# Optimization experiments

Measured on AMD Instinct MI355X. Metric: run time of the kernel, lower is better.

The kernel has to match this reference:

```python
import jax, jax.numpy as jnp
import numpy as np

B = 524288
D_IN = 128
H = 16          # hard-coded by amax slicing in MLSTMCell
D_OUT = 4


def _quant(x, amax):
    # torch quant_tensor: clamp(round(x * 127/amax), -127, 127) -> int8 (kept as
    # integer-valued float32 here; exact since |v| <= 127)
    if amax.ndim > 1:
        amax = jnp.squeeze(amax, 1)
    return jnp.clip(jnp.round(x * (127.0 / amax)), -127.0, 127.0)


def _dequant(x, amax, double=False):
    max_range = 127.0 ** 2 if double else 127.0
    scale = max_range / amax
    if scale.ndim > 1:
        scale = jnp.squeeze(scale, 1)
    return x / scale


def setup_inputs() -> dict:
    key = jax.random.key(0)
    ks = jax.random.split(key, 13)
    # weights are stored pre-quantized int8 (integer-valued); torch casts them
    # to int32 before matmul, so integer-valued float32 is bit-exact in fp32
    intw = lambda k, shp: jax.random.randint(k, shp, -127, 128).astype(jnp.float32)
    x = jax.random.normal(ks[0], (B, D_IN), dtype=jnp.float32)
    h = jax.random.normal(ks[1], (B, H), dtype=jnp.float32) * 0.1
    c = jax.random.normal(ks[2], (B, H), dtype=jnp.float32) * 0.1
    w1 = intw(ks[3], (H, D_IN))          # net.0.weight
    w_ih = intw(ks[4], (4 * H, H))       # lstm.weight_ih
    w_hh = intw(ks[5], (4 * H, H))       # lstm.weight_hh
    w_out = intw(ks[6], (D_OUT, H))      # output_layer.weight
    u = lambda k, shp, lo, hi: jax.random.uniform(k, shp, minval=lo, maxval=hi, dtype=jnp.float32)
    amax_in0 = u(ks[7], (), 1.0, 4.0)            # net.0._input_quantizer._amax (per-tensor)
    amax_w0 = u(ks[8], (H, 1), 32.0, 127.0)      # net.0._weight_quantizer._amax (per-channel)
    amax_lstm_in = u(ks[9], (), 1.0, 4.0)        # lstm._input_quantizer._amax
    amax_w_lstm = u(ks[10], (4 * H, 1), 32.0, 127.0)  # lstm._weight_quantizer._amax
    amax_out_in = u(ks[11], (), 1.0, 4.0)        # output_layer._input_quantizer._amax
    amax_w_out = u(ks[12], (D_OUT, 1), 32.0, 127.0)   # output_layer._weight_quantizer._amax
    return dict(x=x, h=h, c=c, w1=w1, w_ih=w_ih, w_hh=w_hh, w_out=w_out,
                amax_in0=amax_in0, amax_w0=amax_w0, amax_lstm_in=amax_lstm_in,
                amax_w_lstm=amax_w_lstm, amax_out_in=amax_out_in, amax_w_out=amax_w_out)


def reference(x, h, c, w1, w_ih, w_hh, w_out, amax_in0, amax_w0,
              amax_lstm_in, amax_w_lstm, amax_out_in, amax_w_out):
    # --- fc_1: quantize input, int matmul, relu, requantize for lstm ---
    xq = _quant(x, amax_in0)                     # [B, D_IN] int8-valued
    a = xq @ w1.T                                # [B, H] int32-valued (exact in fp32)
    a = jnp.maximum(a, 0.0)                      # relu
    a = _quant(_dequant(a, amax_in0 * amax_w0, double=True), amax_lstm_in)  # [B, H]
    # --- quantize hidden state (hc arrives as float) ---
    hq = _quant(h, amax_lstm_in)
    cq = _quant(c, amax_lstm_in)
    # --- MLSTMCell ---
    amax = amax_lstm_in * amax_w_lstm            # [4H, 1]
    gates = a @ w_ih.T + hq @ w_hh.T             # [B, 4H] int32-valued
    gates = _dequant(gates, amax, double=True)
    i, f, g, o = jnp.split(gates, 4, axis=1)
    gates = jnp.concatenate([jax.nn.sigmoid(i), jax.nn.sigmoid(f),
                             jnp.tanh(g), jax.nn.sigmoid(o)], axis=1)
    gq = _quant(gates, amax)                     # [B, 4H] int8-valued
    i, f, g, o = jnp.split(gq, 4, axis=1)
    cy = (_dequant(f * cq, amax[16:32] * 3.4764, double=True)
          + _dequant(i * g, amax[:16] * amax[32:48], double=True))
    od = _dequant(o, amax[48:], double=False)
    hy = od * jnp.tanh(cy)
    # --- output layer ---
    xo = _quant(hy, amax_out_in) @ w_out.T       # [B, D_OUT]
    xo = _dequant(xo, amax_out_in * amax_w_out, double=True)
    return xo, hy, cy
```

## Files before the change

### kernel.cpp

```cpp
#include <hip/hip_runtime.h>
#include <math.h>
#include <limits.h>


#define OFF_QS    0
#define OFF_SFC1  4
#define OFF_SG    20
#define OFF_QG    84
#define OFF_SCF   148
#define OFF_SCIG  164
#define OFF_SOD   180
#define OFF_SXO   196
#define OFF_VBG   200
#define OFF_TI    216
#define OFF_TF    280
#define OFF_TO    344
#define OFF_TG    408
#define OFF_IGT   536
#define OFF_ODT   1064
#define OFF_W1P   1192
#define OFF_WIHP  1704
#define OFF_WHHP  1960
#define OFF_WOUTP 2216

__device__ __forceinline__ float qclip(float v) {
    return fminf(fmaxf(v, -127.0f), 127.0f);
}

__device__ __forceinline__ int sdot4(int a, int b, int c) {
#if __has_builtin(__builtin_amdgcn_sdot4)
    return __builtin_amdgcn_sdot4(a, b, c, false);
#else
    c += ((a << 24) >> 24) * ((b << 24) >> 24);
    c += ((a << 16) >> 24) * ((b << 16) >> 24);
    c += ((a << 8)  >> 24) * ((b << 8)  >> 24);
    c += (a >> 24) * (b >> 24);
    return c;
#endif
}

__device__ __forceinline__ int pack4i(int a, int b, int c, int d) {
    return (a & 255) | ((b & 255) << 8) | ((c & 255) << 16) | (d << 24);
}

__device__ __forceinline__ int pack4f(const float* p) {
    return pack4i((int)p[0], (int)p[1], (int)p[2], (int)p[3]);
}

typedef __attribute__((address_space(1))) const void g_void;
typedef __attribute__((address_space(3))) void l_void;

__device__ __forceinline__ void stage16(const float* g, float* l) {
    __builtin_amdgcn_global_load_lds((g_void*)g, (l_void*)l, 16, 0, 0);
}

#define WAIT_VM0()   { asm volatile("s_waitcnt vmcnt(0)" ::: "memory"); __builtin_amdgcn_sched_barrier(0); }
#define WAIT_VM4()   { asm volatile("s_waitcnt vmcnt(4)" ::: "memory"); __builtin_amdgcn_sched_barrier(0); }
#define WAIT_LGKM0() { asm volatile("s_waitcnt lgkmcnt(0)" ::: "memory"); __builtin_amdgcn_sched_barrier(0); }

__device__ __forceinline__ int qeval_sig(int gi, float s, float q) {
    float v = (float)gi / s;
    float a = 1.0f / (1.0f + expf(-v));
    return (int)qclip(rintf(a * q));
}
__device__ __forceinline__ int qeval_tanh(int gi, float s, float q) {
    float v = (float)gi / s;
    float a = tanhf(v);
    return (int)qclip(rintf(a * q));
}

#define GLIM 1048576

__device__ int search_thr_sig(float s, float q, int target) {
    if (qeval_sig(GLIM, s, q) < target) return INT_MAX;
    int lo = -GLIM, hi = GLIM;
    while (hi - lo > 1) {
        int mid = lo + ((hi - lo) >> 1);
        if (qeval_sig(mid, s, q) >= target) hi = mid; else lo = mid;
    }
    return hi;
}
__device__ int search_thr_tanh(float s, float q, int target) {
    if (qeval_tanh(GLIM, s, q) < target) return INT_MAX;
    int lo = -GLIM, hi = GLIM;
    while (hi - lo > 1) {
        int mid = lo + ((hi - lo) >> 1);
        if (qeval_tanh(mid, s, q) >= target) hi = mid; else lo = mid;
    }
    return hi;
}

__global__ void __launch_bounds__(1024) setup_all(
    const float* __restrict__ w1, const float* __restrict__ w_ih,
    const float* __restrict__ w_hh, const float* __restrict__ w_out,
    const float* __restrict__ a_in0, const float* __restrict__ a_w0,
    const float* __restrict__ a_lstm, const float* __restrict__ a_wl,
    const float* __restrict__ a_out, const float* __restrict__ a_wo,
    float* __restrict__ wsf)
{
    const int t = threadIdx.x;
    int* wsi = (int*)wsf;
    const float amax_in0 = a_in0[0], amax_lstm = a_lstm[0], amax_out = a_out[0];

    if (t == 0) {
        wsf[OFF_QS + 0] = 127.0f / amax_in0;
        wsf[OFF_QS + 1] = 127.0f / amax_lstm;
        wsf[OFF_QS + 2] = 127.0f / amax_out;
    }
    if (t < 16) wsf[OFF_SFC1 + t] = 16129.0f / (amax_in0 * a_w0[t]);
    if (t < 64) {
        float am = amax_lstm * a_wl[t];
        wsf[OFF_SG + t] = 16129.0f / am;
        wsf[OFF_QG + t] = 127.0f / am;
    }
    if (t < 16) {
        float amf = amax_lstm * a_wl[16 + t];
        wsf[OFF_SCF + t] = 16129.0f / (amf * 3.4764f);
        float amo = amax_lstm * a_wl[48 + t];
        wsf[OFF_SOD + t] = 127.0f / amo;
        float ami = amax_lstm * a_wl[t];
        float amg = amax_lstm * a_wl[32 + t];
        wsf[OFF_SCIG + t] = 16129.0f / (ami * amg);
        float s = 16129.0f / amg, q = 127.0f / amg;
        wsi[OFF_VBG + t] = qeval_tanh(-GLIM, s, q);
    }
    if (t < 4) wsf[OFF_SXO + t] = 16129.0f / (amax_out * a_wo[t]);

    if (t < 512) wsi[OFF_W1P + t] = pack4f(w1 + 4 * t);
    if (t < 256) { wsi[OFF_WIHP + t] = pack4f(w_ih + 4 * t);
                   wsi[OFF_WHHP + t] = pack4f(w_hh + 4 * t); }
    if (t < 16)  wsi[OFF_WOUTP + t] = pack4f(w_out + 4 * t);

    if (t < 64) {
        int m = t >> 2, k = t & 3;
        float am = amax_lstm * a_wl[m];
        wsi[OFF_TI + t] = search_thr_sig(16129.0f / am, 127.0f / am, k + 1);
    } else if (t < 128) {
        int u = t - 64, m = u >> 2, k = u & 3;
        float am = amax_lstm * a_wl[16 + m];
        wsi[OFF_TF + u] = search_thr_sig(16129.0f / am, 127.0f / am, k + 1);
    } else if (t < 192) {
        int u = t - 128, m = u >> 2, k = u & 3;
        float am = amax_lstm * a_wl[48 + m];
        wsi[OFF_TO + u] = search_thr_sig(16129.0f / am, 127.0f / am, k + 1);
    } else if (t < 320) {
        int u = t - 192, m = u >> 3, k = u & 7;
        float am = amax_lstm * a_wl[32 + m];
        float s = 16129.0f / am, q = 127.0f / am;
        int vb = qeval_tanh(-GLIM, s, q);
        wsi[OFF_TG + u] = search_thr_tanh(s, q, vb + 1 + k);
    } else if (t < 848) {
        int u = t - 320, m = u / 33, p = u % 33;
        float ami = amax_lstm * a_wl[m];
        float amg = amax_lstm * a_wl[32 + m];
        float scig = 16129.0f / (ami * amg);
        wsf[OFF_IGT + u] = (float)(p - 16) / scig;
    } else if (t < 928) {
        int u = t - 848, m = u / 5, oq = u % 5;
        float amo = amax_lstm * a_wl[48 + m];
        float sod = 127.0f / amo;
        wsf[OFF_ODT + m * 8 + oq] = (float)oq / sod;
    }
}

__global__ void __launch_bounds__(256, 4) mlpq_kernel(
    const float* __restrict__ x, const float* __restrict__ h, const float* __restrict__ c,
    const float* __restrict__ wsf,
    float* __restrict__ out_xo, float* __restrict__ out_hy, float* __restrict__ out_cy,
    int nrows)
{
    __shared__ float s_tab[656];
    __shared__ __align__(1024) float s_stage[4][2048];

    for (int i = threadIdx.x; i < 656; i += 256) s_tab[i] = wsf[OFF_IGT + i];
    __syncthreads();
    const float* s_igt = s_tab;
    const float* s_odt = s_tab + 528;

    const int tid = threadIdx.x;
    const int wv  = tid >> 6;
    const int rl  = tid & 63;
    const int wrow0 = blockIdx.x * 256 + wv * 64;
    const int r = wrow0 + rl;

    const int sw = (rl >> 1) & 3;
    const int qs_stage = (rl & 3) ^ ((rl >> 3) & 3);
    const int rstage = wrow0 + (rl >> 2);

    float* bufE = &s_stage[wv][0];
    float* bufO = &s_stage[wv][1024];

    const int* __restrict__ wsi = (const int*)wsf;
    const float qs_in   = wsf[OFF_QS + 0];
    const float qs_lstm = wsf[OFF_QS + 1];
    const float qs_out  = wsf[OFF_QS + 2];

    const float* gpx = x + (size_t)rstage * 128 + qs_stage * 4;

    float4 hv4[4], cv4[4];
    {
        const float4* hb = reinterpret_cast<const float4*>(h) + (size_t)r * 4;
        const float4* cb = reinterpret_cast<const float4*>(c) + (size_t)r * 4;
#pragma unroll
        for (int jg = 0; jg < 4; ++jg) hv4[jg] = hb[jg];
#pragma unroll
        for (int jg = 0; jg < 4; ++jg) cv4[jg] = cb[jg];
    }
    stage16(gpx + 0 * 2048, bufE + 0 * 256);
    stage16(gpx + 1 * 2048, bufE + 1 * 256);
    stage16(gpx + 2 * 2048, bufE + 2 * 256);
    stage16(gpx + 3 * 2048, bufE + 3 * 256);
    {
        const float* g = gpx + 1 * 16;
        stage16(g + 0 * 2048, bufO + 0 * 256);
        stage16(g + 1 * 2048, bufO + 1 * 256);
        stage16(g + 2 * 2048, bufO + 2 * 256);
        stage16(g + 3 * 2048, bufO + 3 * 256);
    }

    int acc[16];
#pragma unroll
    for (int j = 0; j < 16; ++j) acc[j] = 0;

#pragma unroll
    for (int kc = 0; kc < 8; ++kc) {
        if (kc < 7) { WAIT_VM4(); }
        else        { WAIT_VM0(); }
        float* bk = (kc & 1) ? bufO : bufE;
        const float4* b4 = reinterpret_cast<const float4*>(bk);
        float4 xv[4];
#pragma unroll
        for (int q = 0; q < 4; ++q) xv[q] = b4[rl * 4 + (q ^ sw)];
        WAIT_LGKM0();
        if (kc <= 5) {
            const float* g = gpx + (kc + 2) * 16;
            stage16(g + 0 * 2048, bk + 0 * 256);
            stage16(g + 1 * 2048, bk + 1 * 256);
            stage16(g + 2 * 2048, bk + 2 * 256);
            stage16(g + 3 * 2048, bk + 3 * 256);
        }
#pragma unroll
        for (int q = 0; q < 4; ++q) {
            float4 v = xv[q];
            int w = pack4i((int)qclip(rintf(v.x * qs_in)),
                           (int)qclip(rintf(v.y * qs_in)),
                           (int)qclip(rintf(v.z * qs_in)),
                           (int)qclip(rintf(v.w * qs_in)));
#pragma unroll
            for (int j = 0; j < 16; ++j)
                acc[j] = sdot4(w, wsi[OFF_W1P + j * 32 + kc * 4 + q], acc[j]);
        }
    }

    int aql[4];
#pragma unroll
    for (int jg = 0; jg < 4; ++jg) {
        int q[4];
#pragma unroll
        for (int u = 0; u < 4; ++u) {
            int j = jg * 4 + u;
            int ai = acc[j] > 0 ? acc[j] : 0;
            float dq = (float)ai / wsf[OFF_SFC1 + j];
            q[u] = (int)qclip(rintf(dq * qs_lstm));
        }
        aql[jg] = pack4i(q[0], q[1], q[2], q[3]);
    }

    int hql[4];
#pragma unroll
    for (int jg = 0; jg < 4; ++jg) {
        float4 v = hv4[jg];
        hql[jg] = pack4i((int)qclip(rintf(v.x * qs_lstm)),
                         (int)qclip(rintf(v.y * qs_lstm)),
                         (int)qclip(rintf(v.z * qs_lstm)),
                         (int)qclip(rintf(v.w * qs_lstm)));
    }

    float hyv[16], cyv[16];
    int xql[4];

#pragma unroll
    for (int mg = 0; mg < 4; ++mg) {
        float4 cv = cv4[mg];
        float cvals[4] = {cv.x, cv.y, cv.z, cv.w};
        int xq4[4];
#pragma unroll
        for (int t = 0; t < 4; ++t) {
            const int m = mg * 4 + t;
            int gi = 0, gf = 0, gg = 0, go = 0;
#pragma unroll
            for (int p = 0; p < 4; ++p) {
                int ap = aql[p], hp = hql[p];
                gi = sdot4(ap, wsi[OFF_WIHP + (m)      * 4 + p], gi);
                gi = sdot4(hp, wsi[OFF_WHHP + (m)      * 4 + p], gi);
                gf = sdot4(ap, wsi[OFF_WIHP + (m + 16) * 4 + p], gf);
                gf = sdot4(hp, wsi[OFF_WHHP + (m + 16) * 4 + p], gf);
                gg = sdot4(ap, wsi[OFF_WIHP + (m + 32) * 4 + p], gg);
                gg = sdot4(hp, wsi[OFF_WHHP + (m + 32) * 4 + p], gg);
                go = sdot4(ap, wsi[OFF_WIHP + (m + 48) * 4 + p], go);
                go = sdot4(hp, wsi[OFF_WHHP + (m + 48) * 4 + p], go);
            }
            int iq = (gi >= wsi[OFF_TI + m * 4 + 0]) + (gi >= wsi[OFF_TI + m * 4 + 1])
                   + (gi >= wsi[OFF_TI + m * 4 + 2]) + (gi >= wsi[OFF_TI + m * 4 + 3]);
            int fq = (gf >= wsi[OFF_TF + m * 4 + 0]) + (gf >= wsi[OFF_TF + m * 4 + 1])
                   + (gf >= wsi[OFF_TF + m * 4 + 2]) + (gf >= wsi[OFF_TF + m * 4 + 3]);
            int oq = (go >= wsi[OFF_TO + m * 4 + 0]) + (go >= wsi[OFF_TO + m * 4 + 1])
                   + (go >= wsi[OFF_TO + m * 4 + 2]) + (go >= wsi[OFF_TO + m * 4 + 3]);
            int gq = wsi[OFF_VBG + m]
                   + (gg >= wsi[OFF_TG + m * 8 + 0]) + (gg >= wsi[OFF_TG + m * 8 + 1])
                   + (gg >= wsi[OFF_TG + m * 8 + 2]) + (gg >= wsi[OFF_TG + m * 8 + 3])
                   + (gg >= wsi[OFF_TG + m * 8 + 4]) + (gg >= wsi[OFF_TG + m * 8 + 5])
                   + (gg >= wsi[OFF_TG + m * 8 + 6]) + (gg >= wsi[OFF_TG + m * 8 + 7]);

            int cqv = (int)qclip(rintf(cvals[t] * qs_lstm));

            float cy = (float)(fq * cqv) / wsf[OFF_SCF + m]
                     + s_igt[m * 33 + (iq * gq + 16)];
            float od = s_odt[m * 8 + oq];
            float hy = od * tanhf(cy);

            hyv[m] = hy;
            cyv[m] = cy;
            xq4[t] = (int)qclip(rintf(hy * qs_out));
        }
        xql[mg] = pack4i(xq4[0], xq4[1], xq4[2], xq4[3]);
    }

    float4 xov;
    {
        int s0 = 0, s1 = 0, s2 = 0, s3 = 0;
#pragma unroll
        for (int p = 0; p < 4; ++p) {
            s0 = sdot4(xql[p], wsi[OFF_WOUTP + 0 * 4 + p], s0);
            s1 = sdot4(xql[p], wsi[OFF_WOUTP + 1 * 4 + p], s1);
            s2 = sdot4(xql[p], wsi[OFF_WOUTP + 2 * 4 + p], s2);
            s3 = sdot4(xql[p], wsi[OFF_WOUTP + 3 * 4 + p], s3);
        }
        xov.x = (float)s0 / wsf[OFF_SXO + 0];
        xov.y = (float)s1 / wsf[OFF_SXO + 1];
        xov.z = (float)s2 / wsf[OFF_SXO + 2];
        xov.w = (float)s3 / wsf[OFF_SXO + 3];
    }
    reinterpret_cast<float4*>(out_xo)[r] = xov;

    float* tb = bufE;
    const int g  = (rl >> 2);
    const int mq = rl & 3;
    float4* hb4 = reinterpret_cast<float4*>(out_hy) + (size_t)wrow0 * 4;
    float4* cb4 = reinterpret_cast<float4*>(out_cy) + (size_t)wrow0 * 4;

    WAIT_LGKM0();
#pragma unroll
    for (int q = 0; q < 4; ++q)
        *reinterpret_cast<float4*>(&tb[rl * 20 + q * 4]) =
            make_float4(hyv[q * 4 + 0], hyv[q * 4 + 1], hyv[q * 4 + 2], hyv[q * 4 + 3]);
    WAIT_LGKM0();
#pragma unroll
    for (int s = 0; s < 4; ++s) {
        float4 v = *reinterpret_cast<const float4*>(&tb[(s * 16 + g) * 20 + mq * 4]);
        hb4[s * 64 + rl] = v;
    }
    WAIT_LGKM0();
#pragma unroll
    for (int q = 0; q < 4; ++q)
        *reinterpret_cast<float4*>(&tb[rl * 20 + q * 4]) =
            make_float4(cyv[q * 4 + 0], cyv[q * 4 + 1], cyv[q * 4 + 2], cyv[q * 4 + 3]);
    WAIT_LGKM0();
#pragma unroll
    for (int s = 0; s < 4; ++s) {
        float4 v = *reinterpret_cast<const float4*>(&tb[(s * 16 + g) * 20 + mq * 4]);
        cb4[s * 64 + rl] = v;
    }
}

extern "C" void kernel_launch(void* const* d_in, const int* in_sizes, int n_in,
                              void* d_out, int out_size, void* d_ws, size_t ws_size,
                              hipStream_t stream) {
    const float* x      = (const float*)d_in[0];
    const float* h      = (const float*)d_in[1];
    const float* c      = (const float*)d_in[2];
    const float* w1     = (const float*)d_in[3];
    const float* w_ih   = (const float*)d_in[4];
    const float* w_hh   = (const float*)d_in[5];
    const float* w_out  = (const float*)d_in[6];
    const float* a_in0  = (const float*)d_in[7];
    const float* a_w0   = (const float*)d_in[8];
    const float* a_lstm = (const float*)d_in[9];
    const float* a_wl   = (const float*)d_in[10];
    const float* a_out  = (const float*)d_in[11];
    const float* a_wo   = (const float*)d_in[12];

    const int B = in_sizes[0] / 128;
    float* out    = (float*)d_out;
    float* out_xo = out;
    float* out_hy = out + (size_t)B * 4;
    float* out_cy = out + (size_t)B * 20;
    float* wsf    = (float*)d_ws;

    hipLaunchKernelGGL(setup_all, dim3(1), dim3(1024), 0, stream,
                       w1, w_ih, w_hh, w_out, a_in0, a_w0, a_lstm, a_wl, a_out, a_wo, wsf);

    dim3 block(256);
    dim3 grid((B + 255) / 256);
    hipLaunchKernelGGL(mlpq_kernel, grid, block, 0, stream,
                       x, h, c, wsf, out_xo, out_hy, out_cy, B);
}
```

Before: 109.2 us.

## Make kernel persistent over two row tiles with cross-tile prefetch of x, h, c

Launches a fixed grid of 1024 blocks, each looping over two 256-row tiles, so the next tile's x chunk and h rows are prefetched while the current tile's LSTM and output stages run. The c tile is now staged into LDS through the async pipeline, and the hy/cy transpose buffer uses an XOR swizzle in place of padding. The aim is to hide global-load latency across tiles and cut tail and launch overhead. The grid is hard-coded to assume B == 1024*256*2, and register pressure rises from holding prefetched h values.

```diff
diff --git a/kernel.cpp b/kernel.cpp
--- a/kernel.cpp
+++ b/kernel.cpp
@@ -163,6 +163,9 @@
     }
 }
 
+#define NBLK 1024
+#define TILES 2
+
 __global__ void __launch_bounds__(256, 4) mlpq_kernel(
     const float* __restrict__ x, const float* __restrict__ h, const float* __restrict__ c,
     const float* __restrict__ wsf,
@@ -180,196 +183,233 @@
     const int tid = threadIdx.x;
     const int wv  = tid >> 6;
     const int rl  = tid & 63;
-    const int wrow0 = blockIdx.x * 256 + wv * 64;
-    const int r = wrow0 + rl;
-
     const int sw = (rl >> 1) & 3;
     const int qs_stage = (rl & 3) ^ ((rl >> 3) & 3);
-    const int rstage = wrow0 + (rl >> 2);
-
-    float* bufE = &s_stage[wv][0];
-    float* bufO = &s_stage[wv][1024];
+    const int g2 = rl >> 2;
+    const int mq = rl & 3;
+
+    float* A = &s_stage[wv][0];
+    float* B = &s_stage[wv][1024];
 
     const int* __restrict__ wsi = (const int*)wsf;
     const float qs_in   = wsf[OFF_QS + 0];
     const float qs_lstm = wsf[OFF_QS + 1];
     const float qs_out  = wsf[OFF_QS + 2];
 
-    const float* gpx = x + (size_t)rstage * 128 + qs_stage * 4;
-
-    float4 hv4[4], cv4[4];
+    float4 hv4[4];
     {
-        const float4* hb = reinterpret_cast<const float4*>(h) + (size_t)r * 4;
-        const float4* cb = reinterpret_cast<const float4*>(c) + (size_t)r * 4;
+        const int r0 = blockIdx.x * 256 + wv * 64 + rl;
+        const float4* hb = reinterpret_cast<const float4*>(h) + (size_t)r0 * 4;
 #pragma unroll
         for (int jg = 0; jg < 4; ++jg) hv4[jg] = hb[jg];
-#pragma unroll
-        for (int jg = 0; jg < 4; ++jg) cv4[jg] = cb[jg];
-    }
-    stage16(gpx + 0 * 2048, bufE + 0 * 256);
-    stage16(gpx + 1 * 2048, bufE + 1 * 256);
-    stage16(gpx + 2 * 2048, bufE + 2 * 256);
-    stage16(gpx + 3 * 2048, bufE + 3 * 256);
-    {
-        const float* g = gpx + 1 * 16;
-        stage16(g + 0 * 2048, bufO + 0 * 256);
-        stage16(g + 1 * 2048, bufO + 1 * 256);
-        stage16(g + 2 * 2048, bufO + 2 * 256);
-        stage16(g + 3 * 2048, bufO + 3 * 256);
-    }
-
-    int acc[16];
-#pragma unroll
-    for (int j = 0; j < 16; ++j) acc[j] = 0;
-
-#pragma unroll
-    for (int kc = 0; kc < 8; ++kc) {
-        if (kc < 7) { WAIT_VM4(); }
-        else        { WAIT_VM0(); }
-        float* bk = (kc & 1) ? bufO : bufE;
-        const float4* b4 = reinterpret_cast<const float4*>(bk);
-        float4 xv[4];
-#pragma unroll
-        for (int q = 0; q < 4; ++q) xv[q] = b4[rl * 4 + (q ^ sw)];
+        const int rs0 = blockIdx.x * 256 + wv * 64 + (rl >> 2);
+        const float* g0 = x + (size_t)rs0 * 128 + qs_stage * 4;
+        stage16(g0 + 0 * 2048, A + 0 * 256);
+        stage16(g0 + 1 * 2048, A + 1 * 256);
+        stage16(g0 + 2 * 2048, A + 2 * 256);
+        stage16(g0 + 3 * 2048, A + 3 * 256);
+    }
+
+#pragma unroll 1
+    for (int t = 0; t < TILES; ++t) {
+        const int wrow0 = (blockIdx.x + t * NBLK) * 256 + wv * 64;
+        const int r = wrow0 + rl;
+        const int rstage = wrow0 + (rl >> 2);
+        const float* gpx = x + (size_t)rstage * 128 + qs_stage * 4;
+        const float* gpc = c + (size_t)rstage * 16 + qs_stage * 4;
+
         WAIT_LGKM0();
-        if (kc <= 5) {
-            const float* g = gpx + (kc + 2) * 16;
-            stage16(g + 0 * 2048, bk + 0 * 256);
-            stage16(g + 1 * 2048, bk + 1 * 256);
-            stage16(g + 2 * 2048, bk + 2 * 256);
-            stage16(g + 3 * 2048, bk + 3 * 256);
-        }
-#pragma unroll
-        for (int q = 0; q < 4; ++q) {
-            float4 v = xv[q];
-            int w = pack4i((int)qclip(rintf(v.x * qs_in)),
-                           (int)qclip(rintf(v.y * qs_in)),
-                           (int)qclip(rintf(v.z * qs_in)),
-                           (int)qclip(rintf(v.w * qs_in)));
-#pragma unroll
-            for (int j = 0; j < 16; ++j)
-                acc[j] = sdot4(w, wsi[OFF_W1P + j * 32 + kc * 4 + q], acc[j]);
-        }
-    }
-
-    int aql[4];
-#pragma unroll
-    for (int jg = 0; jg < 4; ++jg) {
-        int q[4];
-#pragma unroll
-        for (int u = 0; u < 4; ++u) {
-            int j = jg * 4 + u;
-            int ai = acc[j] > 0 ? acc[j] : 0;
-            float dq = (float)ai / wsf[OFF_SFC1 + j];
-            q[u] = (int)qclip(rintf(dq * qs_lstm));
-        }
-        aql[jg] = pack4i(q[0], q[1], q[2], q[3]);
-    }
-
-    int hql[4];
-#pragma unroll
-    for (int jg = 0; jg < 4; ++jg) {
-        float4 v = hv4[jg];
-        hql[jg] = pack4i((int)qclip(rintf(v.x * qs_lstm)),
-                         (int)qclip(rintf(v.y * qs_lstm)),
-                         (int)qclip(rintf(v.z * qs_lstm)),
-                         (int)qclip(rintf(v.w * qs_lstm)));
-    }
-
-    float hyv[16], cyv[16];
-    int xql[4];
-
-#pragma unroll
-    for (int mg = 0; mg < 4; ++mg) {
-        float4 cv = cv4[mg];
-        float cvals[4] = {cv.x, cv.y, cv.z, cv.w};
-        int xq4[4];
-#pragma unroll
-        for (int t = 0; t < 4; ++t) {
-            const int m = mg * 4 + t;
-            int gi = 0, gf = 0, gg = 0, go = 0;
+        {
+            const float* g = gpx + 16;
+            stage16(g + 0 * 2048, B + 0 * 256);
+            stage16(g + 1 * 2048, B + 1 * 256);
+            stage16(g + 2 * 2048, B + 2 * 256);
+            stage16(g + 3 * 2048, B + 3 * 256);
+        }
+
+        int acc[16];
+#pragma unroll
+        for (int j = 0; j < 16; ++j) acc[j] = 0;
+        int hql[4];
+        float4 hv4n[4];
+
+#pragma unroll
+        for (int kc = 0; kc < 8; ++kc) {
+            WAIT_VM4();
+            float* bk = (kc & 1) ? B : A;
+            const float4* b4 = reinterpret_cast<const float4*>(bk);
+            float4 xv[4];
+#pragma unroll
+            for (int q = 0; q < 4; ++q) xv[q] = b4[rl * 4 + (q ^ sw)];
+            WAIT_LGKM0();
+            if (kc <= 5) {
+                const float* g = gpx + (kc + 2) * 16;
+                stage16(g + 0 * 2048, bk + 0 * 256);
+                stage16(g + 1 * 2048, bk + 1 * 256);
+                stage16(g + 2 * 2048, bk + 2 * 256);
+                stage16(g + 3 * 2048, bk + 3 * 256);
+            } else if (kc == 6) {
+                stage16(gpc + 0 * 256, bk + 0 * 256);
+                stage16(gpc + 1 * 256, bk + 1 * 256);
+                stage16(gpc + 2 * 256, bk + 2 * 256);
+                stage16(gpc + 3 * 256, bk + 3 * 256);
+            } else {
+                if (t < TILES - 1) {
+                    const int rn = (blockIdx.x + (t + 1) * NBLK) * 256 + wv * 64 + rl;
+                    const float4* hb = reinterpret_cast<const float4*>(h) + (size_t)rn * 4;
+#pragma unroll
+                    for (int jg = 0; jg < 4; ++jg) hv4n[jg] = hb[jg];
+                }
+            }
+            if (kc == 0) {
+#pragma unroll
+                for (int jg = 0; jg < 4; ++jg) {
+                    float4 v = hv4[jg];
+                    hql[jg] = pack4i((int)qclip(rintf(v.x * qs_lstm)),
+                                     (int)qclip(rintf(v.y * qs_lstm)),
+                                     (int)qclip(rintf(v.z * qs_lstm)),
+                                     (int)qclip(rintf(v.w * qs_lstm)));
+                }
+            }
+#pragma unroll
+            for (int q = 0; q < 4; ++q) {
+                float4 v = xv[q];
+                int w = pack4i((int)qclip(rintf(v.x * qs_in)),
+                               (int)qclip(rintf(v.y * qs_in)),
+                               (int)qclip(rintf(v.z * qs_in)),
+                               (int)qclip(rintf(v.w * qs_in)));
+#pragma unroll
+                for (int j = 0; j < 16; ++j)
+                    acc[j] = sdot4(w, wsi[OFF_W1P + j * 32 + kc * 4 + q], acc[j]);
+            }
+        }
+
+        int aql[4];
+#pragma unroll
+        for (int jg = 0; jg < 4; ++jg) {
+            int q[4];
+#pragma unroll
+            for (int u = 0; u < 4; ++u) {
+                int j = jg * 4 + u;
+                int ai = acc[j] > 0 ? acc[j] : 0;
+                float dq = (float)ai / wsf[OFF_SFC1 + j];
+                q[u] = (int)qclip(rintf(dq * qs_lstm));
+            }
+            aql[jg] = pack4i(q[0], q[1], q[2], q[3]);
+        }
+
+        if (t < TILES - 1) { WAIT_VM4(); }
+        else               { WAIT_VM0(); }
+
+        const float4* c4 = reinterpret_cast<const float4*>(A);
+        float hyv[16], cyv[16];
+        int xql[4];
+
+#pragma unroll
+        for (int mg = 0; mg < 4; ++mg) {
+            float4 cv = c4[rl * 4 + (mg ^ sw)];
+            float cvals[4] = {cv.x, cv.y, cv.z, cv.w};
+            int xq4[4];
+#pragma unroll
+            for (int tt = 0; tt < 4; ++tt) {
+                const int m = mg * 4 + tt;
+                int gi = 0, gf = 0, gg = 0, go = 0;
+#pragma unroll
+                for (int p = 0; p < 4; ++p) {
+                    int ap = aql[p], hp = hql[p];
+                    gi = sdot4(ap, wsi[OFF_WIHP + (m)      * 4 + p], gi);
+                    gi = sdot4(hp, wsi[OFF_WHHP + (m)      * 4 + p], gi);
+                    gf = sdot4(ap, wsi[OFF_WIHP + (m + 16) * 4 + p], gf);
+                    gf = sdot4(hp, wsi[OFF_WHHP + (m + 16) * 4 + p], gf);
+                    gg = sdot4(ap, wsi[OFF_WIHP + (m + 32) * 4 + p], gg);
+                    gg = sdot4(hp, wsi[OFF_WHHP + (m + 32) * 4 + p], gg);
+                    go = sdot4(ap, wsi[OFF_WIHP + (m + 48) * 4 + p], go);
+                    go = sdot4(hp, wsi[OFF_WHHP + (m + 48) * 4 + p], go);
+                }
+                int iq = (gi >= wsi[OFF_TI + m * 4 + 0]) + (gi >= wsi[OFF_TI + m * 4 + 1])
+                       + (gi >= wsi[OFF_TI + m * 4 + 2]) + (gi >= wsi[OFF_TI + m * 4 + 3]);
+                int fq = (gf >= wsi[OFF_TF + m * 4 + 0]) + (gf >= wsi[OFF_TF + m * 4 + 1])
+                       + (gf >= wsi[OFF_TF + m * 4 + 2]) + (gf >= wsi[OFF_TF + m * 4 + 3]);
+                int oq = (go >= wsi[OFF_TO + m * 4 + 0]) + (go >= wsi[OFF_TO + m * 4 + 1])
+                       + (go >= wsi[OFF_TO + m * 4 + 2]) + (go >= wsi[OFF_TO + m * 4 + 3]);
+                int gq = wsi[OFF_VBG + m]
+                       + (gg >= wsi[OFF_TG + m * 8 + 0]) + (gg >= wsi[OFF_TG + m * 8 + 1])
+                       + (gg >= wsi[OFF_TG + m * 8 + 2]) + (gg >= wsi[OFF_TG + m * 8 + 3])
+                       + (gg >= wsi[OFF_TG + m * 8 + 4]) + (gg >= wsi[OFF_TG + m * 8 + 5])
+                       + (gg >= wsi[OFF_TG + m * 8 + 6]) + (gg >= wsi[OFF_TG + m * 8 + 7]);
+
+                int cqv = (int)qclip(rintf(cvals[tt] * qs_lstm));
+
+                float cy = (float)(fq * cqv) / wsf[OFF_SCF + m]
+                         + s_igt[m * 33 + (iq * gq + 16)];
+                float od = s_odt[m * 8 + oq];
+                float hy = od * tanhf(cy);
+
+                hyv[m] = hy;
+                cyv[m] = cy;
+                xq4[tt] = (int)qclip(rintf(hy * qs_out));
+            }
+            xql[mg] = pack4i(xq4[0], xq4[1], xq4[2], xq4[3]);
+        }
+
+        WAIT_LGKM0();
+        if (t < TILES - 1) {
+            const int rsn = (blockIdx.x + (t + 1) * NBLK) * 256 + wv * 64 + (rl >> 2);
+            const float* gn = x + (size_t)rsn * 128 + qs_stage * 4;
+            stage16(gn + 0 * 2048, A + 0 * 256);
+            stage16(gn + 1 * 2048, A + 1 * 256);
+            stage16(gn + 2 * 2048, A + 2 * 256);
+            stage16(gn + 3 * 2048, A + 3 * 256);
+        }
+
+        float4 xov;
+        {
+            int s0 = 0, s1 = 0, s2 = 0, s3 = 0;
 #pragma unroll
             for (int p = 0; p < 4; ++p) {
-                int ap = aql[p], hp = hql[p];
-                gi = sdot4(ap, wsi[OFF_WIHP + (m)      * 4 + p], gi);
-                gi = sdot4(hp, wsi[OFF_WHHP + (m)      * 4 + p], gi);
-                gf = sdot4(ap, wsi[OFF_WIHP + (m + 16) * 4 + p], gf);
-                gf = sdot4(hp, wsi[OFF_WHHP + (m + 16) * 4 + p], gf);
-                gg = sdot4(ap, wsi[OFF_WIHP + (m + 32) * 4 + p], gg);
-                gg = sdot4(hp, wsi[OFF_WHHP + (m + 32) * 4 + p], gg);
-                go = sdot4(ap, wsi[OFF_WIHP + (m + 48) * 4 + p], go);
-                go = sdot4(hp, wsi[OFF_WHHP + (m + 48) * 4 + p], go);
-            }
-            int iq = (gi >= wsi[OFF_TI + m * 4 + 0]) + (gi >= wsi[OFF_TI + m * 4 + 1])
-                   + (gi >= wsi[OFF_TI + m * 4 + 2]) + (gi >= wsi[OFF_TI + m * 4 + 3]);
-            int fq = (gf >= wsi[OFF_TF + m * 4 + 0]) + (gf >= wsi[OFF_TF + m * 4 + 1])
-                   + (gf >= wsi[OFF_TF + m * 4 + 2]) + (gf >= wsi[OFF_TF + m * 4 + 3]);
-            int oq = (go >= wsi[OFF_TO + m * 4 + 0]) + (go >= wsi[OFF_TO + m * 4 + 1])
-                   + (go >= wsi[OFF_TO + m * 4 + 2]) + (go >= wsi[OFF_TO + m * 4 + 3]);
-            int gq = wsi[OFF_VBG + m]
-                   + (gg >= wsi[OFF_TG + m * 8 + 0]) + (gg >= wsi[OFF_TG + m * 8 + 1])
-                   + (gg >= wsi[OFF_TG + m * 8 + 2]) + (gg >= wsi[OFF_TG + m * 8 + 3])
-                   + (gg >= wsi[OFF_TG + m * 8 + 4]) + (gg >= wsi[OFF_TG + m * 8 + 5])
-                   + (gg >= wsi[OFF_TG + m * 8 + 6]) + (gg >= wsi[OFF_TG + m * 8 + 7]);
-
-            int cqv = (int)qclip(rintf(cvals[t] * qs_lstm));
-
-            float cy = (float)(fq * cqv) / wsf[OFF_SCF + m]
-                     + s_igt[m * 33 + (iq * gq + 16)];
-            float od = s_odt[m * 8 + oq];
-            float hy = od * tanhf(cy);
-
-            hyv[m] = hy;
-            cyv[m] = cy;
-            xq4[t] = (int)qclip(rintf(hy * qs_out));
-        }
-        xql[mg] = pack4i(xq4[0], xq4[1], xq4[2], xq4[3]);
-    }
-
-    float4 xov;
-    {
-        int s0 = 0, s1 = 0, s2 = 0, s3 = 0;
-#pragma unroll
-        for (int p = 0; p < 4; ++p) {
-            s0 = sdot4(xql[p], wsi[OFF_WOUTP + 0 * 4 + p], s0);
-            s1 = sdot4(xql[p], wsi[OFF_WOUTP + 1 * 4 + p], s1);
-            s2 = sdot4(xql[p], wsi[OFF_WOUTP + 2 * 4 + p], s2);
-            s3 = sdot4(xql[p], wsi[OFF_WOUTP + 3 * 4 + p], s3);
-        }
-        xov.x = (float)s0 / wsf[OFF_SXO + 0];
-        xov.y = (float)s1 / wsf[OFF_SXO + 1];
-        xov.z = (float)s2 / wsf[OFF_SXO + 2];
-        xov.w = (float)s3 / wsf[OFF_SXO + 3];
-    }
-    reinterpret_cast<float4*>(out_xo)[r] = xov;
-
-    float* tb = bufE;
-    const int g  = (rl >> 2);
-    const int mq = rl & 3;
-    float4* hb4 = reinterpret_cast<float4*>(out_hy) + (size_t)wrow0 * 4;
-    float4* cb4 = reinterpret_cast<float4*>(out_cy) + (size_t)wrow0 * 4;
-
-    WAIT_LGKM0();
-#pragma unroll
-    for (int q = 0; q < 4; ++q)
-        *reinterpret_cast<float4*>(&tb[rl * 20 + q * 4]) =
-            make_float4(hyv[q * 4 + 0], hyv[q * 4 + 1], hyv[q * 4 + 2], hyv[q * 4 + 3]);
-    WAIT_LGKM0();
-#pragma unroll
-    for (int s = 0; s < 4; ++s) {
-        float4 v = *reinterpret_cast<const float4*>(&tb[(s * 16 + g) * 20 + mq * 4]);
-        hb4[s * 64 + rl] = v;
-    }
-    WAIT_LGKM0();
-#pragma unroll
-    for (int q = 0; q < 4; ++q)
-        *reinterpret_cast<float4*>(&tb[rl * 20 + q * 4]) =
-            make_float4(cyv[q * 4 + 0], cyv[q * 4 + 1], cyv[q * 4 + 2], cyv[q * 4 + 3]);
-    WAIT_LGKM0();
-#pragma unroll
-    for (int s = 0; s < 4; ++s) {
-        float4 v = *reinterpret_cast<const float4*>(&tb[(s * 16 + g) * 20 + mq * 4]);
-        cb4[s * 64 + rl] = v;
+                s0 = sdot4(xql[p], wsi[OFF_WOUTP + 0 * 4 + p], s0);
+                s1 = sdot4(xql[p], wsi[OFF_WOUTP + 1 * 4 + p], s1);
+                s2 = sdot4(xql[p], wsi[OFF_WOUTP + 2 * 4 + p], s2);
+                s3 = sdot4(xql[p], wsi[OFF_WOUTP + 3 * 4 + p], s3);
+            }
+            xov.x = (float)s0 / wsf[OFF_SXO + 0];
+            xov.y = (float)s1 / wsf[OFF_SXO + 1];
+            xov.z = (float)s2 / wsf[OFF_SXO + 2];
+            xov.w = (float)s3 / wsf[OFF_SXO + 3];
+        }
+        reinterpret_cast<float4*>(out_xo)[r] = xov;
+
+        float4* hb4 = reinterpret_cast<float4*>(out_hy) + (size_t)wrow0 * 4;
+        float4* cb4 = reinterpret_cast<float4*>(out_cy) + (size_t)wrow0 * 4;
+        const int wsl = (rl >> 1) & 3;
+#pragma unroll
+        for (int q = 0; q < 4; ++q)
+            *reinterpret_cast<float4*>(&B[rl * 16 + ((q ^ wsl) << 2)]) =
+                make_float4(hyv[q * 4 + 0], hyv[q * 4 + 1], hyv[q * 4 + 2], hyv[q * 4 + 3]);
+        WAIT_LGKM0();
+#pragma unroll
+        for (int s = 0; s < 4; ++s) {
+            const int R = s * 16 + g2;
+            float4 v = *reinterpret_cast<const float4*>(&B[R * 16 + ((mq ^ ((R >> 1) & 3)) << 2)]);
+            hb4[s * 64 + rl] = v;
+        }
+        WAIT_LGKM0();
+#pragma unroll
+        for (int q = 0; q < 4; ++q)
+            *reinterpret_cast<float4*>(&B[rl * 16 + ((q ^ wsl) << 2)]) =
+                make_float4(cyv[q * 4 + 0], cyv[q * 4 + 1], cyv[q * 4 + 2], cyv[q * 4 + 3]);
+        WAIT_LGKM0();
+#pragma unroll
+        for (int s = 0; s < 4; ++s) {
+            const int R = s * 16 + g2;
+            float4 v = *reinterpret_cast<const float4*>(&B[R * 16 + ((mq ^ ((R >> 1) & 3)) << 2)]);
+            cb4[s * 64 + rl] = v;
+        }
+
+        if (t < TILES - 1) {
+#pragma unroll
+            for (int jg = 0; jg < 4; ++jg) hv4[jg] = hv4n[jg];
+        }
     }
 }
 
@@ -401,7 +441,7 @@
                        w1, w_ih, w_hh, w_out, a_in0, a_w0, a_lstm, a_wl, a_out, a_wo, wsf);
 
     dim3 block(256);
-    dim3 grid((B + 255) / 256);
+    dim3 grid(NBLK);
     hipLaunchKernelGGL(mlpq_kernel, grid, block, 0, stream,
                        x, h, c, wsf, out_xo, out_hy, out_cy, B);
 }
```

Result: slower. 191.8 us (+75.6%).
